# Kernel optimization log

Hardware: AMD Instinct MI355X
Metric: run time of the kernel (lower is better)

## Reference

```python
import jax, jax.numpy as jnp
import numpy as np

B, T, C = 8, 1024, 2048
N_HEAD = 16
HEAD = C // N_HEAD  # 128


def setup_inputs() -> dict:
    key = jax.random.key(0)
    k1, k2, k3 = jax.random.split(key, 3)
    scale = 0.02
    x = jax.random.normal(k1, (B, T, C), dtype=jnp.float32)
    W_attn = jax.random.normal(k2, (C, 3 * C), dtype=jnp.float32) * scale
    b_attn = jnp.zeros((3 * C,), dtype=jnp.float32)
    W_proj = jax.random.normal(k3, (C, C), dtype=jnp.float32) * scale
    b_proj = jnp.zeros((C,), dtype=jnp.float32)
    return {"x": x, "W_attn": W_attn, "b_attn": b_attn, "W_proj": W_proj, "b_proj": b_proj}


def reference(x, W_attn, b_attn, W_proj, b_proj):
    Bq, Tq, Cq = x.shape
    qkv = x @ W_attn + b_attn                       # [B,T,3C]
    q, k, v = jnp.split(qkv, 3, axis=2)             # each [B,T,C]
    def heads(t):
        return t.reshape(Bq, Tq, N_HEAD, HEAD).transpose(0, 2, 1, 3)  # [B,H,T,D]
    q, k, v = heads(q), heads(k), heads(v)
    scores = jnp.einsum('bhqd,bhkd->bhqk', q, k) / jnp.sqrt(jnp.float32(HEAD))
    causal = jnp.tril(jnp.ones((Tq, Tq), dtype=bool))
    scores = jnp.where(causal, scores, jnp.float32(-1e9))
    attn = jax.nn.softmax(scores, axis=-1)          # [B,H,T,T]
    y = jnp.einsum('bhqk,bhkd->bhqd', attn, v)      # [B,H,T,D]
    y = y.transpose(0, 2, 1, 3).reshape(Bq, Tq, Cq) # [B,T,C]
    return y @ W_proj + b_proj
```

## Files before the change

kernel.cpp:

```cpp
#include <hip/hip_runtime.h>
#include <hip/hip_bf16.h>


typedef unsigned short u16;
typedef __bf16 bf16x8 __attribute__((ext_vector_type(8)));
typedef float f32x4 __attribute__((ext_vector_type(4)));

#define B_ 8
#define T_ 1024
#define C_ 2048
#define NH 16
#define HD 128
#define BH (B_*NH)

__device__ __forceinline__ u16 f2b(float f){
  __bf16 h = (__bf16)f; return __builtin_bit_cast(u16, h);
}
__device__ __forceinline__ unsigned pk2(float x, float y){
  return (unsigned)f2b(x) | ((unsigned)f2b(y) << 16);
}
__device__ __forceinline__ bf16x8 ldfrag(const u16* p){
  uint4 u = *(const uint4*)p; return __builtin_bit_cast(bf16x8, u);
}
__device__ __forceinline__ void glds16(const u16* g, const u16* l){
  __builtin_amdgcn_global_load_lds(
      (const __attribute__((address_space(1))) void*)g,
      (__attribute__((address_space(3))) void*)l, 16, 0, 0);
}
__device__ __forceinline__ void sbar(){
  __builtin_amdgcn_sched_barrier(0);
  __builtin_amdgcn_s_barrier();
  __builtin_amdgcn_sched_barrier(0);
}

__global__ __launch_bounds__(256) void prep(
    const float* __restrict__ W_attn, u16* __restrict__ Wat,
    const float* __restrict__ W_proj, u16* __restrict__ Wpt,
    const float4* __restrict__ x4, ushort4* __restrict__ xb4, int do_cvt)
{
  __shared__ u16 tile[64][65];
  const int t = threadIdx.x;
  const int z = blockIdx.z;
  if (z == 1 && blockIdx.x >= 32){
    if (!do_cvt) return;
    const int n4 = (B_*T_*C_)/4;
    int i = ((blockIdx.x - 32)*32 + blockIdx.y)*256 + t;
    const int stride = 2048*256;
    for (; i < n4; i += stride){
      float4 f = x4[i];
      ushort4 o; o.x = f2b(f.x); o.y = f2b(f.y); o.z = f2b(f.z); o.w = f2b(f.w);
      xb4[i] = o;
    }
    return;
  }
  const float* in = (z == 0) ? W_attn : W_proj;
  u16* outp       = (z == 0) ? Wat    : Wpt;
  const int R = 2048, C = (z == 0) ? 6144 : 2048;
  const int r0 = blockIdx.y * 64, c0 = blockIdx.x * 64;
#pragma unroll
  for (int ii = 0; ii < 16; ++ii){
    int idx = t + ii*256; int r = idx >> 6, c = idx & 63;
    tile[r][c] = f2b(in[(size_t)(r0 + r)*C + c0 + c]);
  }
  __syncthreads();
#pragma unroll
  for (int ii = 0; ii < 16; ++ii){
    int idx = t + ii*256; int r = idx >> 6, c = idx & 63;
    outp[(size_t)(c0 + r)*R + r0 + c] = tile[c][r];
  }
}

__device__ __forceinline__ void qkv_epilogue(
    const f32x4 acc[4][4], const float* bias, int bx, int by,
    int wm, int wn, int lq, int ln,
    u16* qb, u16* kb, u16* vb)
{
  const int tensor = bx >> 4, h = bx & 15, b = by >> 3, t0 = (by & 7)*128;
  u16* tb = tensor==0 ? qb : (tensor==1 ? kb : vb);
  u16* op = tb + ((size_t)(b*NH + h)*T_ + t0)*HD;
#pragma unroll
  for (int j=0;j<4;j++){
    const float bv = bias[bx*128 + wn*64 + j*16 + ln];
    const int n = wn*64 + j*16 + ln;
#pragma unroll
    for (int i=0;i<4;i++){
      const int m0 = wm*64 + i*16 + lq*4;
#pragma unroll
      for (int r=0;r<4;r++)
        op[(size_t)(m0 + r)*HD + n] = f2b(acc[i][j][r] + bv);
    }
  }
}

__global__ __launch_bounds__(512,2) void gemm_qkv_8p(
    const u16* __restrict__ Xb, const u16* __restrict__ Wt,
    const float* __restrict__ bias,
    u16* __restrict__ qb, u16* __restrict__ kb, u16* __restrict__ vb)
{
  __shared__ u16 lds[2][2][256*64];
  const int t = threadIdx.x;
  const int lane = t & 63, wid = t >> 6;
  const int lq = lane >> 4, ln = lane & 15;
  const int wm = wid >> 2, wn = wid & 3;

  const int bid0 = blockIdx.x;
  const int bid = (bid0 & 7)*96 + (bid0 >> 3);
  const int bx = bid % 24, by = bid / 24;

  const int rl  = (wid << 4) + (lane >> 3);
  const int sw0 = (lane & 7) ^ (rl & 7);
  const u16* Ag = Xb + ((size_t)(by*256) + rl)*2048;
  const u16* Bg = Wt + ((size_t)(bx*256) + rl)*2048;
  const size_t q0off = (size_t)sw0*8;
  const size_t q1off = (size_t)8*2048 + (size_t)sw0*8;

#define STAGE(buf_, op_, h_, T_) do { \
    const u16* s_ = (op_ ? Bg : Ag) + (size_t)(h_)*(128*2048) + (size_t)(T_)*64; \
    const u16* d_ = &lds[buf_][op_][(((h_)*128) + (wid<<4))*64]; \
    glds16(s_ + q0off, d_); \
    glds16(s_ + q1off, d_ + 8*64); \
  } while(0)

  const int swr0 = (0*4 + lq) ^ (ln & 7);
  const int swr1 = (1*4 + lq) ^ (ln & 7);

  const f32x4 fz = {0.f,0.f,0.f,0.f};
  f32x4 acc[8][4];
#pragma unroll
  for (int f=0;f<8;f++)
#pragma unroll
    for (int g=0;g<4;g++) acc[f][g] = fz;

  STAGE(0,0,0,0); STAGE(0,0,1,0); STAGE(0,1,0,0); STAGE(0,1,1,0);
  STAGE(1,1,0,1); STAGE(1,1,1,1); STAGE(1,0,0,1);
  asm volatile("s_waitcnt vmcnt(6)" ::: "memory");
  sbar();

  for (int T = 0; T < 32; ++T){
    const int b = T & 1;
    const u16* As = lds[b][0];
    const u16* Bs = lds[b][1];
    bf16x8 a0[4][2], a4[4][2], bfr[4][2];

#pragma unroll
    for (int f=0;f<4;f++){
      a0[f][0]  = ldfrag(&As[(wm*128 + f*16 + ln)*64 + swr0*8]);
      a0[f][1]  = ldfrag(&As[(wm*128 + f*16 + ln)*64 + swr1*8]);
      bfr[f][0] = ldfrag(&Bs[(wn*64  + f*16 + ln)*64 + swr0*8]);
      bfr[f][1] = ldfrag(&Bs[(wn*64  + f*16 + ln)*64 + swr1*8]);
    }
    if (T+1 < 32) STAGE(b^1, 0, 1, T+1);
    sbar();
    __builtin_amdgcn_s_setprio(1);
#pragma unroll
    for (int f=0;f<4;f++)
#pragma unroll
      for (int g=0;g<2;g++){
        acc[f][g] = __builtin_amdgcn_mfma_f32_16x16x32_bf16(a0[f][0], bfr[g][0], acc[f][g], 0,0,0);
        acc[f][g] = __builtin_amdgcn_mfma_f32_16x16x32_bf16(a0[f][1], bfr[g][1], acc[f][g], 0,0,0);
      }
    __builtin_amdgcn_s_setprio(0);
    sbar();

#pragma unroll
    for (int f=0;f<4;f++){
      a4[f][0] = ldfrag(&As[(wm*128 + (f+4)*16 + ln)*64 + swr0*8]);
      a4[f][1] = ldfrag(&As[(wm*128 + (f+4)*16 + ln)*64 + swr1*8]);
    }
    if (T+2 < 32) STAGE(b, 1, 0, T+2);
    sbar();
    __builtin_amdgcn_s_setprio(1);
#pragma unroll
    for (int f=0;f<4;f++)
#pragma unroll
      for (int g=0;g<2;g++){
        acc[f+4][g] = __builtin_amdgcn_mfma_f32_16x16x32_bf16(a4[f][0], bfr[g][0], acc[f+4][g], 0,0,0);
        acc[f+4][g] = __builtin_amdgcn_mfma_f32_16x16x32_bf16(a4[f][1], bfr[g][1], acc[f+4][g], 0,0,0);
      }
    __builtin_amdgcn_s_setprio(0);
    sbar();

    if (T+2 < 32) STAGE(b, 1, 1, T+2);
    sbar();
    __builtin_amdgcn_s_setprio(1);
#pragma unroll
    for (int f=0;f<4;f++)
#pragma unroll
      for (int g=2;g<4;g++){
        acc[f+4][g] = __builtin_amdgcn_mfma_f32_16x16x32_bf16(a4[f][0], bfr[g][0], acc[f+4][g], 0,0,0);
        acc[f+4][g] = __builtin_amdgcn_mfma_f32_16x16x32_bf16(a4[f][1], bfr[g][1], acc[f+4][g], 0,0,0);
      }
    __builtin_amdgcn_s_setprio(0);
    sbar();

    if (T+2 < 32) STAGE(b, 0, 0, T+2);
    if (T >= 30) asm volatile("s_waitcnt vmcnt(0)" ::: "memory");
    else         asm volatile("s_waitcnt vmcnt(6)" ::: "memory");
    sbar();
    __builtin_amdgcn_s_setprio(1);
#pragma unroll
    for (int f=0;f<4;f++)
#pragma unroll
      for (int g=2;g<4;g++){
        acc[f][g] = __builtin_amdgcn_mfma_f32_16x16x32_bf16(a0[f][0], bfr[g][0], acc[f][g], 0,0,0);
        acc[f][g] = __builtin_amdgcn_mfma_f32_16x16x32_bf16(a0[f][1], bfr[g][1], acc[f][g], 0,0,0);
      }
    __builtin_amdgcn_s_setprio(0);
    sbar();
  }
#undef STAGE

  const int tensor = bx >> 3;
  u16* tb = tensor==0 ? qb : (tensor==1 ? kb : vb);
  const int m_base = by*256 + wm*128;
#pragma unroll
  for (int g=0; g<4; ++g){
    const int ncol = (bx & 7)*256 + wn*64 + g*16 + ln;
    const float bv = bias[tensor*2048 + ncol];
    const int h = ncol >> 7, d = ncol & 127;
#pragma unroll
    for (int f=0; f<8; ++f){
      const int m0 = m_base + f*16 + lq*4;
      const int bb = m0 >> 10, tt = m0 & 1023;
      u16* op = tb + ((size_t)(bb*NH + h)*T_ + tt)*HD + d;
#pragma unroll
      for (int r=0;r<4;++r)
        op[(size_t)r*HD] = f2b(acc[f][g][r] + bv);
    }
  }
}

__global__ __launch_bounds__(512,2) void gemm_proj_8p(
    const u16* __restrict__ Y, const u16* __restrict__ Wt,
    const float* __restrict__ bias, float* __restrict__ outp)
{
  __shared__ u16 lds[2][2][256*64];
  const int t = threadIdx.x;
  const int lane = t & 63, wid = t >> 6;
  const int lq = lane >> 4, ln = lane & 15;
  const int wm = wid >> 2, wn = wid & 3;

  const int bid0 = blockIdx.x;
  const int bid = (bid0 & 7)*32 + (bid0 >> 3);
  const int bx = bid & 7, by = bid >> 3;

  const int rl  = (wid << 4) + (lane >> 3);
  const int sw0 = (lane & 7) ^ (rl & 7);
  const u16* Bg = Wt + ((size_t)(bx*256) + rl)*2048;
  const size_t bq0 = (size_t)sw0*8;
  const size_t arow0 = ((size_t)(by >> 2)*16)*1024 + (size_t)(by & 3)*256 + rl;

#define STAGEP(buf_, op_, h_, Tt_) do { \
    const u16* d_ = &lds[buf_][op_][(((h_)*128) + (wid<<4))*64]; \
    if (op_){ \
      const u16* s_ = Bg + (size_t)(h_)*(128*2048) + (size_t)(Tt_)*64; \
      glds16(s_ + bq0, d_); \
      glds16(s_ + (size_t)8*2048 + bq0, d_ + 8*64); \
    } else { \
      const u16* s_ = Y + (arow0 + (size_t)((Tt_) >> 1)*1024 + (size_t)(h_)*128)*128 \
                        + ((Tt_) & 1)*64 + sw0*8; \
      glds16(s_, d_); \
      glds16(s_ + 8*128, d_ + 8*64); \
    } \
  } while(0)

  const int swr0 = (0*4 + lq) ^ (ln & 7);
  const int swr1 = (1*4 + lq) ^ (ln & 7);

  const f32x4 fz = {0.f,0.f,0.f,0.f};
  f32x4 acc[8][4];
#pragma unroll
  for (int f=0;f<8;f++)
#pragma unroll
    for (int g=0;g<4;g++) acc[f][g] = fz;

  STAGEP(0,0,0,0); STAGEP(0,0,1,0); STAGEP(0,1,0,0); STAGEP(0,1,1,0);
  STAGEP(1,1,0,1); STAGEP(1,1,1,1); STAGEP(1,0,0,1);
  asm volatile("s_waitcnt vmcnt(6)" ::: "memory");
  sbar();

  for (int T = 0; T < 32; ++T){
    const int b = T & 1;
    const u16* As = lds[b][0];
    const u16* Bs = lds[b][1];
    bf16x8 a0[4][2], a4[4][2], bfr[4][2];

#pragma unroll
    for (int f=0;f<4;f++){
      a0[f][0]  = ldfrag(&As[(wm*128 + f*16 + ln)*64 + swr0*8]);
      a0[f][1]  = ldfrag(&As[(wm*128 + f*16 + ln)*64 + swr1*8]);
      bfr[f][0] = ldfrag(&Bs[(wn*64  + f*16 + ln)*64 + swr0*8]);
      bfr[f][1] = ldfrag(&Bs[(wn*64  + f*16 + ln)*64 + swr1*8]);
    }
    if (T+1 < 32) STAGEP(b^1, 0, 1, T+1);
    sbar();
    __builtin_amdgcn_s_setprio(1);
#pragma unroll
    for (int f=0;f<4;f++)
#pragma unroll
      for (int g=0;g<2;g++){
        acc[f][g] = __builtin_amdgcn_mfma_f32_16x16x32_bf16(a0[f][0], bfr[g][0], acc[f][g], 0,0,0);
        acc[f][g] = __builtin_amdgcn_mfma_f32_16x16x32_bf16(a0[f][1], bfr[g][1], acc[f][g], 0,0,0);
      }
    __builtin_amdgcn_s_setprio(0);
    sbar();

#pragma unroll
    for (int f=0;f<4;f++){
      a4[f][0] = ldfrag(&As[(wm*128 + (f+4)*16 + ln)*64 + swr0*8]);
      a4[f][1] = ldfrag(&As[(wm*128 + (f+4)*16 + ln)*64 + swr1*8]);
    }
    if (T+2 < 32) STAGEP(b, 1, 0, T+2);
    sbar();
    __builtin_amdgcn_s_setprio(1);
#pragma unroll
    for (int f=0;f<4;f++)
#pragma unroll
      for (int g=0;g<2;g++){
        acc[f+4][g] = __builtin_amdgcn_mfma_f32_16x16x32_bf16(a4[f][0], bfr[g][0], acc[f+4][g], 0,0,0);
        acc[f+4][g] = __builtin_amdgcn_mfma_f32_16x16x32_bf16(a4[f][1], bfr[g][1], acc[f+4][g], 0,0,0);
      }
    __builtin_amdgcn_s_setprio(0);
    sbar();

    if (T+2 < 32) STAGEP(b, 1, 1, T+2);
    sbar();
    __builtin_amdgcn_s_setprio(1);
#pragma unroll
    for (int f=0;f<4;f++)
#pragma unroll
      for (int g=2;g<4;g++){
        acc[f+4][g] = __builtin_amdgcn_mfma_f32_16x16x32_bf16(a4[f][0], bfr[g][0], acc[f+4][g], 0,0,0);
        acc[f+4][g] = __builtin_amdgcn_mfma_f32_16x16x32_bf16(a4[f][1], bfr[g][1], acc[f+4][g], 0,0,0);
      }
    __builtin_amdgcn_s_setprio(0);
    sbar();

    if (T+2 < 32) STAGEP(b, 0, 0, T+2);
    if (T >= 30) asm volatile("s_waitcnt vmcnt(0)" ::: "memory");
    else         asm volatile("s_waitcnt vmcnt(6)" ::: "memory");
    sbar();
    __builtin_amdgcn_s_setprio(1);
#pragma unroll
    for (int f=0;f<4;f++)
#pragma unroll
      for (int g=2;g<4;g++){
        acc[f][g] = __builtin_amdgcn_mfma_f32_16x16x32_bf16(a0[f][0], bfr[g][0], acc[f][g], 0,0,0);
        acc[f][g] = __builtin_amdgcn_mfma_f32_16x16x32_bf16(a0[f][1], bfr[g][1], acc[f][g], 0,0,0);
      }
    __builtin_amdgcn_s_setprio(0);
    sbar();
  }
#undef STAGEP

  const int m_base = by*256 + wm*128;
#pragma unroll
  for (int g=0; g<4; ++g){
    const int ncol = bx*256 + wn*64 + g*16 + ln;
    const float bv = bias[ncol];
#pragma unroll
    for (int f=0; f<8; ++f){
      const int m0 = m_base + f*16 + lq*4;
      float* op = outp + (size_t)m0*2048 + ncol;
#pragma unroll
      for (int r=0;r<4;++r)
        op[(size_t)r*2048] = acc[f][g][r] + bv;
    }
  }
}

__global__ __launch_bounds__(256,2) void gemm_qkv_f32(
    const float* __restrict__ X, const u16* __restrict__ Wt, const float* __restrict__ bias,
    u16* __restrict__ qb, u16* __restrict__ kb, u16* __restrict__ vb)
{
  __shared__ u16 As[128*32];
  __shared__ u16 Bs[128*32];
  const int t = threadIdx.x;
  const int bx = blockIdx.x, by = blockIdx.y;
  const int lane = t & 63, wv = t >> 6;
  const int lq = lane >> 4, ln = lane & 15;
  const int wm = wv >> 1, wn = wv & 1;

  const int ar = t >> 1, ah = t & 1;
  const float* Ap = X + (size_t)(by*128 + ar)*2048 + ah*16;
  u16* AsW = &As[ar*32 + ah*16];

  const int c0 = t, c1 = 256 + t;
  const u16* Bp0 = Wt + (size_t)(bx*128 + (c0 >> 2))*2048 + (c0 & 3)*8;
  const u16* Bp1 = Wt + (size_t)(bx*128 + (c1 >> 2))*2048 + (c1 & 3)*8;
  const u16* BsW0 = &Bs[(wv*64)*8];
  const u16* BsW1 = &Bs[(256 + wv*64)*8];

  const f32x4 fz = {0.f,0.f,0.f,0.f};
  f32x4 acc[4][4];
#pragma unroll
  for (int i=0;i<4;i++)
#pragma unroll
    for (int j=0;j<4;j++) acc[i][j] = fz;

  for (int kt = 0; kt < 64; ++kt){
    float4 a0 = *(const float4*)(Ap);
    float4 a1 = *(const float4*)(Ap + 4);
    float4 a2 = *(const float4*)(Ap + 8);
    float4 a3 = *(const float4*)(Ap + 12);
    Ap += 32;
    __syncthreads();
    uint4 w0, w1;
    w0.x = pk2(a0.x,a0.y); w0.y = pk2(a0.z,a0.w);
    w0.z = pk2(a1.x,a1.y); w0.w = pk2(a1.z,a1.w);
    w1.x = pk2(a2.x,a2.y); w1.y = pk2(a2.z,a2.w);
    w1.z = pk2(a3.x,a3.y); w1.w = pk2(a3.z,a3.w);
    *(uint4*)(AsW) = w0; *(uint4*)(AsW + 8) = w1;
    glds16(Bp0, BsW0);
    glds16(Bp1, BsW1);
    Bp0 += 32; Bp1 += 32;
    __syncthreads();
    bf16x8 af[4], bf[4];
#pragma unroll
    for (int i=0;i<4;i++) af[i] = ldfrag(&As[(wm*64 + i*16 + ln)*32 + lq*8]);
#pragma unroll
    for (int j=0;j<4;j++) bf[j] = ldfrag(&Bs[(wn*64 + j*16 + ln)*32 + lq*8]);
#pragma unroll
    for (int i=0;i<4;i++)
#pragma unroll
      for (int j=0;j<4;j++)
        acc[i][j] = __builtin_amdgcn_mfma_f32_16x16x32_bf16(af[i], bf[j], acc[i][j], 0,0,0);
  }
  qkv_epilogue(acc, bias, bx, by, wm, wn, lq, ln, qb, kb, vb);
}

__global__ __launch_bounds__(256,2) void attn_fwd(
    u16* qy, const u16* __restrict__ kk, const u16* __restrict__ vv)
{
  __shared__ u16 Ks[2][64*128];
  __shared__ u16 Vt[2][128*64];
  __shared__ u16 Ps[4*32*64];
  const int qt = 7 - blockIdx.x, bh = blockIdx.y;
  const int t = threadIdx.x;
  const int lane = t & 63, wv = t >> 6;
  const int lq = lane >> 4, ln = lane & 15;

  bf16x8 qf[2][4];
#pragma unroll
  for (int i=0;i<2;i++)
#pragma unroll
    for (int kc=0;kc<4;kc++){
      int qrow = qt*128 + wv*32 + i*16 + ln;
      qf[i][kc] = ldfrag(&qy[((size_t)bh*T_ + qrow)*HD + kc*32 + lq*8]);
    }

  const f32x4 fz = {0.f,0.f,0.f,0.f};
  f32x4 o[2][8];
#pragma unroll
  for (int i=0;i<2;i++)
#pragma unroll
    for (int jd=0;jd<8;jd++) o[i][jd] = fz;
  float mi[2][4], li[2][4];
#pragma unroll
  for (int i=0;i<2;i++)
#pragma unroll
    for (int r=0;r<4;r++){ mi[i][r] = -1e30f; li[i][r] = 0.f; }

  const float scale = 0.08838834764831843f;
  const int kr = t & 63, dbase = (t >> 6)*32;
  const int nkt = 2*qt + 2;

  uint4 kreg[4];
  uint4 vreg[4];
  {
    const uint4* ksrc = (const uint4*)(kk + (size_t)bh*T_*HD);
#pragma unroll
    for (int ii=0; ii<4; ++ii) kreg[ii] = ksrc[t + ii*256];
#pragma unroll
    for (int ch=0; ch<4; ++ch)
      vreg[ch] = *(const uint4*)&vv[((size_t)bh*T_ + kr)*HD + dbase + ch*8];
  }

  for (int kt = 0; kt < nkt; ++kt){
    const int b = kt & 1;
    uint4* kdst = (uint4*)Ks[b];
#pragma unroll
    for (int ii=0; ii<4; ++ii){
      const int c = t + ii*256;
      kdst[(c & ~15) | ((c & 15) ^ ((c >> 4) & 7))] = kreg[ii];
    }
#pragma unroll
    for (int ch=0; ch<4; ++ch){
      const u16* e = (const u16*)&vreg[ch];
#pragma unroll
      for (int j=0; j<8; ++j){
        const int d = dbase + ch*8 + j;
        Vt[b][d*64 + (kr ^ ((d & 7) << 3))] = e[j];
      }
    }
    {
      const int ktn = (kt+1 < nkt) ? kt+1 : kt;
      const uint4* ksrc = (const uint4*)(kk + ((size_t)bh*T_ + ktn*64)*HD);
#pragma unroll
      for (int ii=0; ii<4; ++ii) kreg[ii] = ksrc[t + ii*256];
#pragma unroll
      for (int ch=0; ch<4; ++ch)
        vreg[ch] = *(const uint4*)&vv[((size_t)bh*T_ + ktn*64 + kr)*HD + dbase + ch*8];
    }
    __syncthreads();

    const bool active = (kt*64) <= (qt*128 + wv*32 + 31);
    if (active){

    f32x4 s[2][4];
#pragma unroll
    for (int i=0;i<2;i++)
#pragma unroll
      for (int j=0;j<4;j++) s[i][j] = fz;
    __builtin_amdgcn_s_setprio(1);
#pragma unroll
    for (int j=0;j<4;j++){
      bf16x8 kf[4];
      const int krow = j*16 + ln;
      const int ksw = (krow & 7) << 3;
#pragma unroll
      for (int kc=0;kc<4;kc++)
        kf[kc] = ldfrag(&Ks[b][krow*128 + ((kc*32 + lq*8) ^ ksw)]);
#pragma unroll
      for (int i=0;i<2;i++)
#pragma unroll
        for (int kc=0;kc<4;kc++)
          s[i][j] = __builtin_amdgcn_mfma_f32_16x16x32_bf16(qf[i][kc], kf[kc], s[i][j], 0,0,0);
    }
    __builtin_amdgcn_s_setprio(0);

#pragma unroll
    for (int i=0;i<2;i++)
#pragma unroll
      for (int j=0;j<4;j++)
#pragma unroll
        for (int r=0;r<4;r++){
          int qg = qt*128 + wv*32 + i*16 + lq*4 + r;
          int kg = kt*64 + j*16 + ln;
          float sv = s[i][j][r]*scale;
          s[i][j][r] = (kg > qg) ? -1e30f : sv;
        }

    float mxv[2][4];
#pragma unroll
    for (int i=0;i<2;i++)
#pragma unroll
      for (int r=0;r<4;r++){
        float mx = fmaxf(fmaxf(s[i][0][r], s[i][1][r]), fmaxf(s[i][2][r], s[i][3][r]));
        mx = fmaxf(mx, __shfl_xor(mx, 1));
        mx = fmaxf(mx, __shfl_xor(mx, 2));
        mx = fmaxf(mx, __shfl_xor(mx, 4));
        mx = fmaxf(mx, __shfl_xor(mx, 8));
        mxv[i][r] = mx;
      }
    bool ok = true;
#pragma unroll
    for (int i=0;i<2;i++)
#pragma unroll
      for (int r=0;r<4;r++) ok = ok && (mxv[i][r] <= mi[i][r] + 8.0f);
    if (!__all((int)ok)){
#pragma unroll
      for (int i=0;i<2;i++)
#pragma unroll
        for (int r=0;r<4;r++){
          float mnew = fmaxf(mi[i][r], mxv[i][r]);
          float alpha = __expf(mi[i][r] - mnew);
          li[i][r] *= alpha;
          mi[i][r] = mnew;
#pragma unroll
          for (int jd=0;jd<8;jd++) o[i][jd][r] *= alpha;
        }
    }
#pragma unroll
    for (int i=0;i<2;i++)
#pragma unroll
      for (int r=0;r<4;r++){
        float rs = 0.f;
#pragma unroll
        for (int j=0;j<4;j++){
          float p = __expf(s[i][j][r] - mi[i][r]);
          s[i][j][r] = p; rs += p;
        }
        rs += __shfl_xor(rs, 1); rs += __shfl_xor(rs, 2);
        rs += __shfl_xor(rs, 4); rs += __shfl_xor(rs, 8);
        li[i][r] += rs;
      }

#pragma unroll
    for (int i=0;i<2;i++)
#pragma unroll
      for (int j=0;j<4;j++)
#pragma unroll
        for (int r=0;r<4;r++){
          const int rr = i*16 + lq*4 + r;
          Ps[wv*2048 + rr*64 + ((j*16 + ln) ^ ((rr & 7) << 3))] = f2b(s[i][j][r]);
        }

    bf16x8 pf[2][2];
#pragma unroll
    for (int i=0;i<2;i++){
      const int prow = i*16 + ln;
      const int psw = (prow & 7) << 3;
#pragma unroll
      for (int kc=0;kc<2;kc++)
        pf[i][kc] = ldfrag(&Ps[wv*2048 + prow*64 + ((kc*32 + lq*8) ^ psw)]);
    }
    __builtin_amdgcn_s_setprio(1);
#pragma unroll
    for (int jd=0;jd<8;jd++){
      const int vrow = jd*16 + ln;
      const int vsw = (vrow & 7) << 3;
#pragma unroll
      for (int kc=0;kc<2;kc++){
        bf16x8 vf = ldfrag(&Vt[b][vrow*64 + ((kc*32 + lq*8) ^ vsw)]);
#pragma unroll
        for (int i=0;i<2;i++)
          o[i][jd] = __builtin_amdgcn_mfma_f32_16x16x32_bf16(pf[i][kc], vf, o[i][jd], 0,0,0);
      }
    }
    __builtin_amdgcn_s_setprio(0);

    }
  }

#pragma unroll
  for (int i=0;i<2;i++)
#pragma unroll
    for (int r=0;r<4;r++){
      float inv = 1.f / li[i][r];
      int row = qt*128 + wv*32 + i*16 + lq*4 + r;
#pragma unroll
      for (int jd=0;jd<8;jd++)
        qy[((size_t)bh*T_ + row)*HD + jd*16 + ln] = f2b(o[i][jd][r] * inv);
    }
}

extern "C" void kernel_launch(void* const* d_in, const int* in_sizes, int n_in,
                              void* d_out, int out_size, void* d_ws, size_t ws_size,
                              hipStream_t stream)
{
  const float* x      = (const float*)d_in[0];
  const float* W_attn = (const float*)d_in[1];
  const float* b_attn = (const float*)d_in[2];
  const float* W_proj = (const float*)d_in[3];
  const float* b_proj = (const float*)d_in[4];
  float* out = (float*)d_out;

  u16* Wat = (u16*)d_ws;
  u16* Wpt = Wat + (size_t)6144*2048;
  u16* qb  = Wpt + (size_t)2048*2048;
  u16* xb  = qb  + (size_t)BH*T_*HD;
  u16* kb  = (u16*)d_out;
  u16* vb  = kb + (size_t)BH*T_*HD;

  const size_t need = ((size_t)6144*2048 + (size_t)2048*2048
                       + 2*(size_t)BH*T_*HD) * sizeof(u16);
  const int big_ws = (ws_size >= need) ? 1 : 0;

  hipLaunchKernelGGL(prep, dim3(96,32,2), dim3(256,1,1), 0, stream,
                     W_attn, Wat, W_proj, Wpt,
                     (const float4*)x, (ushort4*)xb, big_ws);
  if (big_ws){
    hipLaunchKernelGGL(gemm_qkv_8p, dim3(768,1,1), dim3(512,1,1), 0, stream,
                       xb, Wat, b_attn, qb, kb, vb);
  } else {
    hipLaunchKernelGGL(gemm_qkv_f32, dim3(48,64,1), dim3(256,1,1), 0, stream,
                       x, Wat, b_attn, qb, kb, vb);
  }
  hipLaunchKernelGGL(attn_fwd, dim3(8,BH,1), dim3(256,1,1), 0, stream,
                     qb, kb, vb);
  hipLaunchKernelGGL(gemm_proj_8p, dim3(256,1,1), dim3(512,1,1), 0, stream,
                     qb, Wpt, b_proj, out);
}
```

Measured before the change: 598.3 us.

## Compute transposed S so P stays in registers, dropping LDS round trip

Swaps the MFMA operand order so each lane holds one query's scores across keys. The softmax probabilities can then be packed directly into bf16 operand fragments for the PV MFMA instead of being written to and reread from shared memory. Row max and sum reductions shrink to two cross-lane shuffles, and the per-row softmax state drops from 8 to 2 values per lane. The V fragments are now read as two 8-byte LDS loads to match the permuted key order, and the output is stored as 8-byte vectors.

After: 569.4 us. -4.8%, faster.

```diff
diff --git a/kernel.cpp b/kernel.cpp
--- a/kernel.cpp
+++ b/kernel.cpp
@@ -3,6 +3,7 @@
 
 
 typedef unsigned short u16;
+typedef unsigned int u32;
 typedef __bf16 bf16x8 __attribute__((ext_vector_type(8)));
 typedef float f32x4 __attribute__((ext_vector_type(4)));
 
@@ -434,7 +435,6 @@
 {
   __shared__ u16 Ks[2][64*128];
   __shared__ u16 Vt[2][128*64];
-  __shared__ u16 Ps[4*32*64];
   const int qt = 7 - blockIdx.x, bh = blockIdx.y;
   const int t = threadIdx.x;
   const int lane = t & 63, wv = t >> 6;
@@ -455,11 +455,7 @@
   for (int i=0;i<2;i++)
 #pragma unroll
     for (int jd=0;jd<8;jd++) o[i][jd] = fz;
-  float mi[2][4], li[2][4];
-#pragma unroll
-  for (int i=0;i<2;i++)
-#pragma unroll
-    for (int r=0;r<4;r++){ mi[i][r] = -1e30f; li[i][r] = 0.f; }
+  float mi[2] = {-1e30f, -1e30f}, li[2] = {0.f, 0.f};
 
   const float scale = 0.08838834764831843f;
   const int kr = t & 63, dbase = (t >> 6)*32;
@@ -525,114 +521,111 @@
       for (int i=0;i<2;i++)
 #pragma unroll
         for (int kc=0;kc<4;kc++)
-          s[i][j] = __builtin_amdgcn_mfma_f32_16x16x32_bf16(qf[i][kc], kf[kc], s[i][j], 0,0,0);
-    }
-    __builtin_amdgcn_s_setprio(0);
-
-#pragma unroll
-    for (int i=0;i<2;i++)
+          s[i][j] = __builtin_amdgcn_mfma_f32_16x16x32_bf16(kf[kc], qf[i][kc], s[i][j], 0,0,0);
+    }
+    __builtin_amdgcn_s_setprio(0);
+
+#pragma unroll
+    for (int i=0;i<2;i++){
+      const int qg = qt*128 + wv*32 + i*16 + ln;
 #pragma unroll
       for (int j=0;j<4;j++)
 #pragma unroll
         for (int r=0;r<4;r++){
-          int qg = qt*128 + wv*32 + i*16 + lq*4 + r;
-          int kg = kt*64 + j*16 + ln;
+          const int kg = kt*64 + j*16 + lq*4 + r;
           float sv = s[i][j][r]*scale;
           s[i][j][r] = (kg > qg) ? -1e30f : sv;
         }
-
-    float mxv[2][4];
-#pragma unroll
-    for (int i=0;i<2;i++)
-#pragma unroll
-      for (int r=0;r<4;r++){
-        float mx = fmaxf(fmaxf(s[i][0][r], s[i][1][r]), fmaxf(s[i][2][r], s[i][3][r]));
-        mx = fmaxf(mx, __shfl_xor(mx, 1));
-        mx = fmaxf(mx, __shfl_xor(mx, 2));
-        mx = fmaxf(mx, __shfl_xor(mx, 4));
-        mx = fmaxf(mx, __shfl_xor(mx, 8));
-        mxv[i][r] = mx;
-      }
-    bool ok = true;
-#pragma unroll
-    for (int i=0;i<2;i++)
-#pragma unroll
-      for (int r=0;r<4;r++) ok = ok && (mxv[i][r] <= mi[i][r] + 8.0f);
+    }
+
+    float mx[2];
+#pragma unroll
+    for (int i=0;i<2;i++){
+      float m = s[i][0][0];
+#pragma unroll
+      for (int j=0;j<4;j++)
+#pragma unroll
+        for (int r=0;r<4;r++) m = fmaxf(m, s[i][j][r]);
+      m = fmaxf(m, __shfl_xor(m, 16));
+      m = fmaxf(m, __shfl_xor(m, 32));
+      mx[i] = m;
+    }
+    bool ok = (mx[0] <= mi[0] + 8.0f) && (mx[1] <= mi[1] + 8.0f);
     if (!__all((int)ok)){
 #pragma unroll
-      for (int i=0;i<2;i++)
+      for (int i=0;i<2;i++){
+        float mnew = fmaxf(mi[i], mx[i]);
+        float alpha = __expf(mi[i] - mnew);
+        li[i] *= alpha;
+        mi[i] = mnew;
+#pragma unroll
+        for (int jd=0;jd<8;jd++)
+#pragma unroll
+          for (int r=0;r<4;r++) o[i][jd][r] *= alpha;
+      }
+    }
+#pragma unroll
+    for (int i=0;i<2;i++){
+      float rs = 0.f;
+#pragma unroll
+      for (int j=0;j<4;j++)
 #pragma unroll
         for (int r=0;r<4;r++){
-          float mnew = fmaxf(mi[i][r], mxv[i][r]);
-          float alpha = __expf(mi[i][r] - mnew);
-          li[i][r] *= alpha;
-          mi[i][r] = mnew;
-#pragma unroll
-          for (int jd=0;jd<8;jd++) o[i][jd][r] *= alpha;
-        }
-    }
-#pragma unroll
-    for (int i=0;i<2;i++)
-#pragma unroll
-      for (int r=0;r<4;r++){
-        float rs = 0.f;
-#pragma unroll
-        for (int j=0;j<4;j++){
-          float p = __expf(s[i][j][r] - mi[i][r]);
+          float p = __expf(s[i][j][r] - mi[i]);
           s[i][j][r] = p; rs += p;
         }
-        rs += __shfl_xor(rs, 1); rs += __shfl_xor(rs, 2);
-        rs += __shfl_xor(rs, 4); rs += __shfl_xor(rs, 8);
-        li[i][r] += rs;
-      }
-
+      rs += __shfl_xor(rs, 16);
+      rs += __shfl_xor(rs, 32);
+      li[i] += rs;
+    }
+
+    bf16x8 pb[2][2];
 #pragma unroll
     for (int i=0;i<2;i++)
 #pragma unroll
-      for (int j=0;j<4;j++)
-#pragma unroll
-        for (int r=0;r<4;r++){
-          const int rr = i*16 + lq*4 + r;
-          Ps[wv*2048 + rr*64 + ((j*16 + ln) ^ ((rr & 7) << 3))] = f2b(s[i][j][r]);
-        }
-
-    bf16x8 pf[2][2];
-#pragma unroll
-    for (int i=0;i<2;i++){
-      const int prow = i*16 + ln;
-      const int psw = (prow & 7) << 3;
-#pragma unroll
-      for (int kc=0;kc<2;kc++)
-        pf[i][kc] = ldfrag(&Ps[wv*2048 + prow*64 + ((kc*32 + lq*8) ^ psw)]);
-    }
+      for (int c=0;c<2;c++){
+        uint4 w;
+        w.x = pk2(s[i][c][0],   s[i][c][1]);
+        w.y = pk2(s[i][c][2],   s[i][c][3]);
+        w.z = pk2(s[i][c+2][0], s[i][c+2][1]);
+        w.w = pk2(s[i][c+2][2], s[i][c+2][3]);
+        pb[i][c] = __builtin_bit_cast(bf16x8, w);
+      }
     __builtin_amdgcn_s_setprio(1);
 #pragma unroll
     for (int jd=0;jd<8;jd++){
       const int vrow = jd*16 + ln;
       const int vsw = (vrow & 7) << 3;
 #pragma unroll
-      for (int kc=0;kc<2;kc++){
-        bf16x8 vf = ldfrag(&Vt[b][vrow*64 + ((kc*32 + lq*8) ^ vsw)]);
+      for (int c=0;c<2;c++){
+        uint2 vlo = *(const uint2*)&Vt[b][vrow*64 + ((c*16     + lq*4) ^ vsw)];
+        uint2 vhi = *(const uint2*)&Vt[b][vrow*64 + (((c+2)*16 + lq*4) ^ vsw)];
+        uint4 vw; vw.x = vlo.x; vw.y = vlo.y; vw.z = vhi.x; vw.w = vhi.y;
+        const bf16x8 va = __builtin_bit_cast(bf16x8, vw);
 #pragma unroll
         for (int i=0;i<2;i++)
-          o[i][jd] = __builtin_amdgcn_mfma_f32_16x16x32_bf16(pf[i][kc], vf, o[i][jd], 0,0,0);
-      }
-    }
-    __builtin_amdgcn_s_setprio(0);
-
-    }
-  }
-
-#pragma unroll
-  for (int i=0;i<2;i++)
-#pragma unroll
-    for (int r=0;r<4;r++){
-      float inv = 1.f / li[i][r];
-      int row = qt*128 + wv*32 + i*16 + lq*4 + r;
-#pragma unroll
-      for (int jd=0;jd<8;jd++)
-        qy[((size_t)bh*T_ + row)*HD + jd*16 + ln] = f2b(o[i][jd][r] * inv);
-    }
+          o[i][jd] = __builtin_amdgcn_mfma_f32_16x16x32_bf16(va, pb[i][c], o[i][jd], 0,0,0);
+      }
+    }
+    __builtin_amdgcn_s_setprio(0);
+
+    }
+  }
+
+#pragma unroll
+  for (int i=0;i<2;i++){
+    const float inv = 1.f / li[i];
+    const int q = qt*128 + wv*32 + i*16 + ln;
+#pragma unroll
+    for (int jd=0;jd<8;jd++){
+      ushort4 w;
+      w.x = f2b(o[i][jd][0] * inv);
+      w.y = f2b(o[i][jd][1] * inv);
+      w.z = f2b(o[i][jd][2] * inv);
+      w.w = f2b(o[i][jd][3] * inv);
+      *(ushort4*)&qy[((size_t)bh*T_ + q)*HD + jd*16 + lq*4] = w;
+    }
+  }
 }
 
 extern "C" void kernel_launch(void* const* d_in, const int* in_sizes, int n_in,
```
